# Performance work log

Measured on AMD Instinct MI355X. Metric: run time of the kernel, lower is better.

The kernel has to match this reference:

```python
import jax, jax.numpy as jnp
import numpy as np


def setup_inputs() -> dict:
    key = jax.random.key(0)
    kx, ks = jax.random.split(key)
    X = jax.random.normal(kx, (8, 4096, 16), dtype=jnp.float32)
    # nn.Parameter(torch.rand(1) + 1.0)
    sigma = jax.random.uniform(ks, (1,), dtype=jnp.float32) + 1.0
    return {"X": X, "sigma": sigma}


def reference(X, sigma):
    sq = jnp.sum(X * X, axis=-1)                       # [B, N]
    inner = jnp.einsum('bnf,bmf->bnm', X, X)           # [B, N, N]
    sqdist = sq[:, :, None] + sq[:, None, :] - 2.0 * inner
    sqdist = jnp.maximum(sqdist, 0.0)                  # guard tiny negatives
    gaussian = jnp.exp(-sqdist / sigma[0])             # [B, N, N]
    # original _softmax: exp(gaussian) / sum over dim 2 == softmax over axis 2
    return jax.nn.softmax(gaussian, axis=2)
```

## Files before the change

kernel.cpp:

```cpp
#include <hip/hip_runtime.h>


typedef float v4f __attribute__((ext_vector_type(4)));
typedef short bf8 __attribute__((ext_vector_type(8)));

constexpr int Bn  = 8;
constexpr int N   = 4096;
constexpr int F   = 16;
constexpr int BM  = 16;
constexpr int BLK = 512;
constexpr int NW  = BLK / 64;
constexpr int NCH = 4;
constexpr int TPC = 8;
constexpr int ROWC = 1024 * 2 + 8;

__device__ __forceinline__ unsigned short f2bf(float x) {
    unsigned int u = __float_as_uint(x);
    unsigned int r = (u + 0x7FFFu + ((u >> 16) & 1u)) >> 16;
    return (unsigned short)r;
}
__device__ __forceinline__ float bf2f(unsigned short h) {
    return __uint_as_float(((unsigned int)h) << 16);
}
__device__ __forceinline__ float uni(float x) {
    return __int_as_float(__builtin_amdgcn_readfirstlane(__float_as_int(x)));
}

__global__ __launch_bounds__(256)
void pack_kernel(const float* __restrict__ X, uint4* __restrict__ Xp,
                 float* __restrict__ sqm) {
    const int b = blockIdx.y;
    const int m = blockIdx.x * 256 + threadIdx.x;
    const float4* src = (const float4*)(X + ((size_t)b * N + m) * F);
    const float4 v0 = src[0], v1 = src[1], v2 = src[2], v3 = src[3];
    const float x[F] = {v0.x, v0.y, v0.z, v0.w, v1.x, v1.y, v1.z, v1.w,
                        v2.x, v2.y, v2.z, v2.w, v3.x, v3.y, v3.z, v3.w};
    float s = 0.f;
    #pragma unroll
    for (int f = 0; f < F; ++f) s = fmaf(x[f], x[f], s);
    sqm[(size_t)b * N + m] = s;

    uint4* dst = Xp + ((size_t)b * N + m) * 4;
    #pragma unroll
    for (int g = 0; g < 4; ++g) {
        unsigned int hi[4], lo[4];
        #pragma unroll
        for (int j = 0; j < 4; ++j) {
            const float xf = x[4 * g + j];
            const unsigned short h = f2bf(xf);
            hi[j] = h;
            lo[j] = f2bf(xf - bf2f(h));
        }
        uint4 c;
        c.x = hi[0] | (hi[1] << 16);
        c.y = hi[2] | (hi[3] << 16);
        c.z = lo[0] | (lo[1] << 16);
        c.w = lo[2] | (lo[3] << 16);
        dst[g] = c;
    }
}

union BfU { uint4 u; bf8 h; };

__global__ __launch_bounds__(BLK, 4)
void gs_mfma(const uint4* __restrict__ Xp, const float* __restrict__ sqm,
             const float* __restrict__ sigma_p, float* __restrict__ out) {
    extern __shared__ char smem[];
    float* red   = (float*)(smem + (size_t)BM * ROWC);
    float* inv16 = red + NW * BM;

    const int tid  = threadIdx.x;
    const int w    = tid >> 6;
    const int lane = tid & 63;
    const int g    = lane >> 4;
    const int cc   = lane & 15;
    const int b    = blockIdx.y;
    const int n0   = blockIdx.x * BM;

    const uint4* Xpb = Xp + (size_t)b * N * 4;
    const float* sqb = sqm + (size_t)b * N;

    BfU b1; b1.u = Xpb[(size_t)(n0 + cc) * 4 + g];
    BfU b2; b2.u = make_uint4(b1.u.z, b1.u.w, b1.u.x, b1.u.y);

    const float sqn_l = sqb[n0 + cc];
    const float nis   = uni(-1.0f / sigma_p[0]);

    unsigned int e_pk[NCH * TPC * 2];
    float psum = 0.f;

    #pragma unroll
    for (int c = 0; c < NCH; ++c) {
        #pragma unroll
        for (int t = 0; t < TPC; ++t) {
            const int m_tile = (c * 64 + w * TPC + t) * 16;
            BfU a; a.u = Xpb[(size_t)(m_tile + cc) * 4 + g];

            v4f acc = {0.f, 0.f, 0.f, 0.f};
            acc = __builtin_amdgcn_mfma_f32_16x16x32_bf16(a.h, b1.h, acc, 0, 0, 0);
            acc = __builtin_amdgcn_mfma_f32_16x16x32_bf16(a.h, b2.h, acc, 0, 0, 0);

            const v4f sm4 = *(const v4f*)(sqb + m_tile + 4 * g);
            float ex = __expf(__expf(fmaxf(fmaf(-2.f, acc.x, sqn_l + sm4.x), 0.f) * nis));
            float ey = __expf(__expf(fmaxf(fmaf(-2.f, acc.y, sqn_l + sm4.y), 0.f) * nis));
            float ez = __expf(__expf(fmaxf(fmaf(-2.f, acc.z, sqn_l + sm4.z), 0.f) * nis));
            float ew = __expf(__expf(fmaxf(fmaf(-2.f, acc.w, sqn_l + sm4.w), 0.f) * nis));

            e_pk[(c * TPC + t) * 2 + 0] = (unsigned int)f2bf(ex) | ((unsigned int)f2bf(ey) << 16);
            e_pk[(c * TPC + t) * 2 + 1] = (unsigned int)f2bf(ez) | ((unsigned int)f2bf(ew) << 16);
            psum += (ex + ey) + (ez + ew);
        }
    }

    psum += __shfl_xor(psum, 16, 64);
    psum += __shfl_xor(psum, 32, 64);
    if (lane < 16) red[w * BM + lane] = psum;
    __syncthreads();
    if (w == 0 && lane < 16) {
        float tot = 0.f;
        #pragma unroll
        for (int w2 = 0; w2 < NW; ++w2) tot += red[w2 * BM + lane];
        inv16[lane] = 1.0f / tot;
    }
    __syncthreads();

    #pragma unroll
    for (int c = 0; c < NCH; ++c) {
        #pragma unroll
        for (int t = 0; t < TPC; ++t) {
            const int gl = (w * TPC + t) * 4 + g;
            uint2 pk;
            pk.x = e_pk[(c * TPC + t) * 2 + 0];
            pk.y = e_pk[(c * TPC + t) * 2 + 1];
            *(uint2*)(smem + (size_t)cc * ROWC + 8 * gl) = pk;
        }
        __syncthreads();

        #pragma unroll
        for (int rsel = 0; rsel < 2; ++rsel) {
            const int rr = w + rsel * NW;
            const float invr = inv16[rr];
            float* rowp = out + ((size_t)b * N + n0 + rr) * (size_t)N + c * 1024;
            #pragma unroll
            for (int k = 0; k < 4; ++k) {
                const int gp = 64 * k + lane;
                const uint2 pk = *(const uint2*)(smem + (size_t)rr * ROWC + 8 * gp);
                v4f v;
                v.x = __uint_as_float(pk.x << 16) * invr;
                v.y = __uint_as_float(pk.x & 0xffff0000u) * invr;
                v.z = __uint_as_float(pk.y << 16) * invr;
                v.w = __uint_as_float(pk.y & 0xffff0000u) * invr;
                ((v4f*)rowp)[gp] = v;
            }
        }
        __syncthreads();
    }
}

extern "C" void kernel_launch(void* const* d_in, const int* in_sizes, int n_in,
                              void* d_out, int out_size, void* d_ws, size_t ws_size,
                              hipStream_t stream) {
    const float* X     = (const float*)d_in[0];
    const float* sigma = (const float*)d_in[1];
    float* out         = (float*)d_out;
    uint4* Xp          = (uint4*)d_ws;
    float* sqm         = (float*)d_ws + (size_t)Bn * N * 16;

    const size_t lds_bytes = (size_t)BM * ROWC + NW * BM * 4 + 16 * 4;
    pack_kernel<<<dim3(N / 256, Bn), 256, 0, stream>>>(X, Xp, sqm);
    gs_mfma<<<dim3(N / BM, Bn), BLK, lds_bytes, stream>>>(Xp, sqm, sigma, out);
}
```

Before: 591.0 us.

## Stage first half of row in LDS directly and use nontemporal output stores

The first half of the 4096 columns now has its exponentials written straight into a doubled LDS staging buffer during compute, and only the second half is held in registers. This cuts register pressure and reduces four chunked LDS-staging and store phases to two, so fewer barriers are needed. Output stores become nontemporal to avoid polluting the cache with the large streaming result, and the per-row inverse sum is made wave-uniform. The larger LDS footprint (about 64 KB per block) may lower occupancy compared with the previous launch bound of 4 blocks.

```diff
diff --git a/kernel.cpp b/kernel.cpp
--- a/kernel.cpp
+++ b/kernel.cpp
@@ -10,9 +10,7 @@
 constexpr int BM  = 16;
 constexpr int BLK = 512;
 constexpr int NW  = BLK / 64;
-constexpr int NCH = 4;
-constexpr int TPC = 8;
-constexpr int ROWC = 1024 * 2 + 8;
+constexpr int ROWC = 2048 * 2 + 8;
 
 __device__ __forceinline__ unsigned short f2bf(float x) {
     unsigned int u = __float_as_uint(x);
@@ -86,30 +84,51 @@
     const float sqn_l = sqb[n0 + cc];
     const float nis   = uni(-1.0f / sigma_p[0]);
 
-    unsigned int e_pk[NCH * TPC * 2];
+    unsigned int e_pk[32];
     float psum = 0.f;
 
     #pragma unroll
-    for (int c = 0; c < NCH; ++c) {
-        #pragma unroll
-        for (int t = 0; t < TPC; ++t) {
-            const int m_tile = (c * 64 + w * TPC + t) * 16;
-            BfU a; a.u = Xpb[(size_t)(m_tile + cc) * 4 + g];
-
-            v4f acc = {0.f, 0.f, 0.f, 0.f};
-            acc = __builtin_amdgcn_mfma_f32_16x16x32_bf16(a.h, b1.h, acc, 0, 0, 0);
-            acc = __builtin_amdgcn_mfma_f32_16x16x32_bf16(a.h, b2.h, acc, 0, 0, 0);
-
-            const v4f sm4 = *(const v4f*)(sqb + m_tile + 4 * g);
-            float ex = __expf(__expf(fmaxf(fmaf(-2.f, acc.x, sqn_l + sm4.x), 0.f) * nis));
-            float ey = __expf(__expf(fmaxf(fmaf(-2.f, acc.y, sqn_l + sm4.y), 0.f) * nis));
-            float ez = __expf(__expf(fmaxf(fmaf(-2.f, acc.z, sqn_l + sm4.z), 0.f) * nis));
-            float ew = __expf(__expf(fmaxf(fmaf(-2.f, acc.w, sqn_l + sm4.w), 0.f) * nis));
-
-            e_pk[(c * TPC + t) * 2 + 0] = (unsigned int)f2bf(ex) | ((unsigned int)f2bf(ey) << 16);
-            e_pk[(c * TPC + t) * 2 + 1] = (unsigned int)f2bf(ez) | ((unsigned int)f2bf(ew) << 16);
-            psum += (ex + ey) + (ez + ew);
-        }
+    for (int t = 0; t < 16; ++t) {
+        const int m_tile = (t * 8 + w) * 16;
+        BfU a; a.u = Xpb[(size_t)(m_tile + cc) * 4 + g];
+
+        v4f acc = {0.f, 0.f, 0.f, 0.f};
+        acc = __builtin_amdgcn_mfma_f32_16x16x32_bf16(a.h, b1.h, acc, 0, 0, 0);
+        acc = __builtin_amdgcn_mfma_f32_16x16x32_bf16(a.h, b2.h, acc, 0, 0, 0);
+
+        const v4f sm4 = *(const v4f*)(sqb + m_tile + 4 * g);
+        float ex = __expf(__expf(fmaxf(fmaf(-2.f, acc.x, sqn_l + sm4.x), 0.f) * nis));
+        float ey = __expf(__expf(fmaxf(fmaf(-2.f, acc.y, sqn_l + sm4.y), 0.f) * nis));
+        float ez = __expf(__expf(fmaxf(fmaf(-2.f, acc.z, sqn_l + sm4.z), 0.f) * nis));
+        float ew = __expf(__expf(fmaxf(fmaf(-2.f, acc.w, sqn_l + sm4.w), 0.f) * nis));
+
+        uint2 pk;
+        pk.x = (unsigned int)f2bf(ex) | ((unsigned int)f2bf(ey) << 16);
+        pk.y = (unsigned int)f2bf(ez) | ((unsigned int)f2bf(ew) << 16);
+        const int gl = (t * 8 + w) * 4 + g;
+        *(uint2*)(smem + (size_t)cc * ROWC + 8 * gl) = pk;
+
+        psum += (ex + ey) + (ez + ew);
+    }
+
+    #pragma unroll
+    for (int t = 0; t < 16; ++t) {
+        const int m_tile = 2048 + (t * 8 + w) * 16;
+        BfU a; a.u = Xpb[(size_t)(m_tile + cc) * 4 + g];
+
+        v4f acc = {0.f, 0.f, 0.f, 0.f};
+        acc = __builtin_amdgcn_mfma_f32_16x16x32_bf16(a.h, b1.h, acc, 0, 0, 0);
+        acc = __builtin_amdgcn_mfma_f32_16x16x32_bf16(a.h, b2.h, acc, 0, 0, 0);
+
+        const v4f sm4 = *(const v4f*)(sqb + m_tile + 4 * g);
+        float ex = __expf(__expf(fmaxf(fmaf(-2.f, acc.x, sqn_l + sm4.x), 0.f) * nis));
+        float ey = __expf(__expf(fmaxf(fmaf(-2.f, acc.y, sqn_l + sm4.y), 0.f) * nis));
+        float ez = __expf(__expf(fmaxf(fmaf(-2.f, acc.z, sqn_l + sm4.z), 0.f) * nis));
+        float ew = __expf(__expf(fmaxf(fmaf(-2.f, acc.w, sqn_l + sm4.w), 0.f) * nis));
+
+        e_pk[t * 2 + 0] = (unsigned int)f2bf(ex) | ((unsigned int)f2bf(ey) << 16);
+        e_pk[t * 2 + 1] = (unsigned int)f2bf(ez) | ((unsigned int)f2bf(ew) << 16);
+        psum += (ex + ey) + (ez + ew);
     }
 
     psum += __shfl_xor(psum, 16, 64);
@@ -125,35 +144,50 @@
     __syncthreads();
 
     #pragma unroll
-    for (int c = 0; c < NCH; ++c) {
-        #pragma unroll
-        for (int t = 0; t < TPC; ++t) {
-            const int gl = (w * TPC + t) * 4 + g;
-            uint2 pk;
-            pk.x = e_pk[(c * TPC + t) * 2 + 0];
-            pk.y = e_pk[(c * TPC + t) * 2 + 1];
-            *(uint2*)(smem + (size_t)cc * ROWC + 8 * gl) = pk;
+    for (int rsel = 0; rsel < 2; ++rsel) {
+        const int r = w + rsel * NW;
+        const float invr = uni(inv16[r]);
+        float* rowp = out + ((size_t)b * N + n0 + r) * (size_t)N;
+        #pragma unroll
+        for (int k = 0; k < 8; ++k) {
+            const int gp = 64 * k + lane;
+            const uint2 pk = *(const uint2*)(smem + (size_t)r * ROWC + 8 * gp);
+            v4f v;
+            v.x = __uint_as_float(pk.x << 16) * invr;
+            v.y = __uint_as_float(pk.x & 0xffff0000u) * invr;
+            v.z = __uint_as_float(pk.y << 16) * invr;
+            v.w = __uint_as_float(pk.y & 0xffff0000u) * invr;
+            __builtin_nontemporal_store(v, (v4f*)rowp + gp);
         }
-        __syncthreads();
-
-        #pragma unroll
-        for (int rsel = 0; rsel < 2; ++rsel) {
-            const int rr = w + rsel * NW;
-            const float invr = inv16[rr];
-            float* rowp = out + ((size_t)b * N + n0 + rr) * (size_t)N + c * 1024;
-            #pragma unroll
-            for (int k = 0; k < 4; ++k) {
-                const int gp = 64 * k + lane;
-                const uint2 pk = *(const uint2*)(smem + (size_t)rr * ROWC + 8 * gp);
-                v4f v;
-                v.x = __uint_as_float(pk.x << 16) * invr;
-                v.y = __uint_as_float(pk.x & 0xffff0000u) * invr;
-                v.z = __uint_as_float(pk.y << 16) * invr;
-                v.w = __uint_as_float(pk.y & 0xffff0000u) * invr;
-                ((v4f*)rowp)[gp] = v;
-            }
+    }
+    __syncthreads();
+
+    #pragma unroll
+    for (int t = 0; t < 16; ++t) {
+        const int gl = (t * 8 + w) * 4 + g;
+        uint2 pk;
+        pk.x = e_pk[t * 2 + 0];
+        pk.y = e_pk[t * 2 + 1];
+        *(uint2*)(smem + (size_t)cc * ROWC + 8 * gl) = pk;
+    }
+    __syncthreads();
+
+    #pragma unroll
+    for (int rsel = 0; rsel < 2; ++rsel) {
+        const int r = w + rsel * NW;
+        const float invr = uni(inv16[r]);
+        float* rowp = out + ((size_t)b * N + n0 + r) * (size_t)N + 2048;
+        #pragma unroll
+        for (int k = 0; k < 8; ++k) {
+            const int gp = 64 * k + lane;
+            const uint2 pk = *(const uint2*)(smem + (size_t)r * ROWC + 8 * gp);
+            v4f v;
+            v.x = __uint_as_float(pk.x << 16) * invr;
+            v.y = __uint_as_float(pk.x & 0xffff0000u) * invr;
+            v.z = __uint_as_float(pk.y << 16) * invr;
+            v.w = __uint_as_float(pk.y & 0xffff0000u) * invr;
+            __builtin_nontemporal_store(v, (v4f*)rowp + gp);
         }
-        __syncthreads();
     }
 }
 
```

After: 536.1 us. -9.3%, faster.
